# Performance work log

Measured on AMD Instinct MI355X. Metric: run time of the kernel, lower is better.

Reference implementation:

```python
import jax, jax.numpy as jnp
import numpy as np

N_NODES = 50000
N_EDGES = 800000
IN_FEATURES = 256
HIDDEN = 128


def setup_inputs() -> dict:
    key = jax.random.key(0)
    k_x, k_r, k_c, k_v, k_w, k_b = jax.random.split(key, 6)
    x = jax.random.normal(k_x, (N_NODES, IN_FEATURES), dtype=jnp.float32)
    adj_row = jax.random.randint(k_r, (N_EDGES,), 0, N_NODES, dtype=jnp.int32)
    adj_col = jax.random.randint(k_c, (N_EDGES,), 0, N_NODES, dtype=jnp.int32)
    adj_val = jax.random.uniform(k_v, (N_EDGES,), dtype=jnp.float32)
    # Linear params: weight [hidden, in_features] (xavier-normal-ish), bias [hidden]
    std = float(np.sqrt(2.0 / (IN_FEATURES + HIDDEN)))
    W = jax.random.normal(k_w, (HIDDEN, IN_FEATURES), dtype=jnp.float32) * std
    b = jax.random.normal(k_b, (HIDDEN,), dtype=jnp.float32) * 0.01
    return {"x": x, "adj_row": adj_row, "adj_col": adj_col, "adj_val": adj_val, "W": W, "b": b}


def reference(x, adj_row, adj_col, adj_val, W, b):
    # support = Linear(x): [N, hidden]
    support = jnp.einsum('nf,hf->nh', x, W) + b
    # sparse adj @ support via edge-list gather + segment-sum scatter
    gathered = support[adj_col] * adj_val[:, None]          # [E, hidden]
    out = jax.ops.segment_sum(gathered, adj_row, num_segments=N_NODES)  # [N, hidden]
    return out
```

## Files before the change

kernel.cpp:

```cpp
#include <hip/hip_runtime.h>

#define N_NODES 50000
#define N_EDGES 800000
#define IN_F    256
#define HIDDEN  128

#define BUCKET_SZ 64
#define NB        782
#define NBINS     1024
#define EBLOCK    3328
#define EPT       13
#define EBLOCKS   241
#define LIN_ROWS  128
#define LBLOCKS   391
#define NTASKS    632
#define OFSP      784
#define CAP       1300

#define SMEM_BYTES 35840

typedef __attribute__((ext_vector_type(8))) short bf16x8;
typedef __attribute__((ext_vector_type(4))) float f32x4;

__device__ inline unsigned short f2bf(float f) {
    unsigned u = __float_as_uint(f);
    u += 0x7FFF + ((u >> 16) & 1);
    return (unsigned short)(u >> 16);
}
__device__ inline bf16x8 cvt8(float4 a, float4 b) {
    bf16x8 r;
    r[0] = (short)f2bf(a.x); r[1] = (short)f2bf(a.y);
    r[2] = (short)f2bf(a.z); r[3] = (short)f2bf(a.w);
    r[4] = (short)f2bf(b.x); r[5] = (short)f2bf(b.y);
    r[6] = (short)f2bf(b.z); r[7] = (short)f2bf(b.w);
    return r;
}
__device__ inline float bfLo(unsigned u) { return __uint_as_float(u << 16); }
__device__ inline float bfHi(unsigned u) { return __uint_as_float(u & 0xFFFF0000u); }

__global__ __launch_bounds__(256) void fused_linear_partition_kernel(
    const float* __restrict__ x, const float* __restrict__ W,
    const float* __restrict__ bias, unsigned short* __restrict__ support,
    const int* __restrict__ adj_row, const int* __restrict__ adj_col,
    const float* __restrict__ adj_val,
    int2* __restrict__ part, int* __restrict__ ofs)
{
    __shared__ __align__(16) char smem[SMEM_BYTES];
    const int tid = threadIdx.x;

    if (blockIdx.x < EBLOCKS) {
        int2* lbuf = (int2*)smem;
        int*  lofs = (int*)(smem + 26624);
        int*  lcur = (int*)(smem + 30720);
        int*  tsum = (int*)(smem + 34816);

        const int task = blockIdx.x;
        const int base = task * EBLOCK;
        const int n    = min(EBLOCK, N_EDGES - base);

        for (int i = tid; i < NBINS; i += 256) lofs[i] = 0;
        __syncthreads();

        unsigned pk[EPT]; float pv[EPT];
#pragma unroll
        for (int i = 0; i < EPT; ++i) {
            int li = tid + i * 256;
            bool ok = li < n;
            int ee = ok ? (base + li) : base;
            int r = adj_row[ee], c = adj_col[ee];
            float v = adj_val[ee];
            if (ok) {
                unsigned bk = (unsigned)r >> 6;
                pk[i] = (bk << 22) | (((unsigned)r & 63u) << 16) | (unsigned)c;
                pv[i] = v;
                atomicAdd(&lofs[bk], 1);
            } else pk[i] = 0xFFFFFFFFu;
        }
        __syncthreads();

        int s0 = lofs[tid * 4], s1 = lofs[tid * 4 + 1];
        int s2 = lofs[tid * 4 + 2], s3 = lofs[tid * 4 + 3];
        int mysum = s0 + s1 + s2 + s3;
        tsum[tid] = mysum;
        __syncthreads();
#pragma unroll
        for (int off = 1; off < 256; off <<= 1) {
            int t = (tid >= off) ? tsum[tid - off] : 0;
            __syncthreads();
            tsum[tid] += t;
            __syncthreads();
        }
        int ex = tsum[tid] - mysum;
        lofs[tid * 4]     = ex;
        lofs[tid * 4 + 1] = ex + s0;
        lofs[tid * 4 + 2] = ex + s0 + s1;
        lofs[tid * 4 + 3] = ex + s0 + s1 + s2;
        __syncthreads();

        for (int i = tid; i < NBINS; i += 256) lcur[i] = lofs[i];
        __syncthreads();

#pragma unroll
        for (int i = 0; i < EPT; ++i) {
            if (pk[i] != 0xFFFFFFFFu) {
                unsigned bk = pk[i] >> 22;
                int p = atomicAdd(&lcur[bk], 1);
                lbuf[p] = make_int2((int)(pk[i] & 0x3FFFFF), __float_as_int(pv[i]));
            }
        }
        __syncthreads();

        for (int j = tid; j < n; j += 256)
            part[(size_t)task * EBLOCK + j] = lbuf[j];
        for (int i = tid; i <= NB; i += 256)
            ofs[(size_t)task * OFSP + i] = lofs[i];
    } else {
        short* wfrag = (short*)smem;

        const int bid  = blockIdx.x - EBLOCKS;
        const int lane = tid & 63;
        const int wave = tid >> 6;
        const int quad = lane >> 4;
        const int l16  = lane & 15;

        int m0 = bid * LIN_ROWS + wave * 32 + l16;
        int m1 = m0 + 16;
        if (m0 >= N_NODES) m0 = N_NODES - 1;
        if (m1 >= N_NODES) m1 = N_NODES - 1;
        const float* xr0 = x + (size_t)m0 * IN_F;
        const float* xr1 = x + (size_t)m1 * IN_F;

        f32x4 acc[2][8];
#pragma unroll
        for (int g = 0; g < 2; ++g)
#pragma unroll
            for (int s = 0; s < 8; ++s) acc[g][s] = (f32x4){0.f, 0.f, 0.f, 0.f};

#pragma unroll
        for (int half = 0; half < 2; ++half) {
#pragma unroll
            for (int it = 0; it < 8; ++it) {
                const int f   = it * 256 + tid;
                const int ln  = f & 63;
                const int s   = (f >> 6) & 7;
                const int kc  = f >> 9;
                const int row = s * 16 + (ln & 15);
                const int k0  = (half * 4 + kc) * 32 + (ln >> 4) * 8;
                const float* wp = W + (size_t)row * IN_F + k0;
                float4 b0 = *(const float4*)wp;
                float4 b1 = *(const float4*)(wp + 4);
                *(bf16x8*)(&wfrag[(size_t)f * 8]) = cvt8(b0, b1);
            }
            __syncthreads();

#pragma unroll
            for (int kc = 0; kc < 4; ++kc) {
                const int k0 = (half * 4 + kc) * 32 + quad * 8;
                float4 a0 = *(const float4*)(xr0 + k0);
                float4 a1 = *(const float4*)(xr0 + k0 + 4);
                bf16x8 af0 = cvt8(a0, a1);
                float4 a2 = *(const float4*)(xr1 + k0);
                float4 a3 = *(const float4*)(xr1 + k0 + 4);
                bf16x8 af1 = cvt8(a2, a3);
                const short* bbase = &wfrag[((size_t)(kc * 8) * 64 + lane) * 8];
#pragma unroll
                for (int s = 0; s < 8; ++s) {
                    bf16x8 bf = *(const bf16x8*)(bbase + (size_t)s * 64 * 8);
                    acc[0][s] = __builtin_amdgcn_mfma_f32_16x16x32_bf16(af0, bf, acc[0][s], 0, 0, 0);
                    acc[1][s] = __builtin_amdgcn_mfma_f32_16x16x32_bf16(af1, bf, acc[1][s], 0, 0, 0);
                }
            }
            __syncthreads();
        }

#pragma unroll
        for (int g = 0; g < 2; ++g) {
            const int rowBase = bid * LIN_ROWS + wave * 32 + g * 16 + quad * 4;
#pragma unroll
            for (int reg = 0; reg < 4; ++reg) {
                const int r = rowBase + reg;
                if (r < N_NODES) {
#pragma unroll
                    for (int s = 0; s < 8; ++s) {
                        const int col = s * 16 + l16;
                        float v = acc[g][s][reg] + bias[col];
                        support[(size_t)r * HIDDEN + col] = f2bf(v);
                    }
                }
            }
        }
    }
}

__global__ __launch_bounds__(512) void bucket_gather_kernel(
    const int* __restrict__ ofs, const int2* __restrict__ part,
    const unsigned int* __restrict__ support_u32, float* __restrict__ out)
{
    __shared__ int2 sbufA[CAP];
    __shared__ int2 sbufB[CAP];
    __shared__ int  sarr[512];
    __shared__ int  hist[BUCKET_SZ];
    __shared__ int  rp[BUCKET_SZ + 1];
    __shared__ int  cur[BUCKET_SZ];

    const int tid  = threadIdx.x;
    const int b    = blockIdx.x;
    const int wave = tid >> 6;
    const int lane = tid & 63;

    if (tid < BUCKET_SZ) hist[tid] = 0;

    int sstart = 0, slen = 0;
    if (tid < EBLOCKS) {
        const int* orow = ofs + (size_t)tid * OFSP + b;
        sstart = orow[0];
        slen   = orow[1] - sstart;
    }
    sarr[tid] = slen;
    __syncthreads();

#pragma unroll
    for (int off = 1; off < 512; off <<= 1) {
        int t = (tid >= off) ? sarr[tid - off] : 0;
        __syncthreads();
        sarr[tid] += t;
        __syncthreads();
    }
    const int excl = sarr[tid] - slen;
    const int n    = min(sarr[511], CAP);

    {
        const int2* seg = part + (size_t)tid * EBLOCK + sstart;
        for (int k = 0; k < slen; ++k) {
            int p = excl + k;
            if (p < CAP) sbufA[p] = seg[k];
        }
    }
    __syncthreads();

    for (int j = tid; j < n; j += 512)
        atomicAdd(&hist[(sbufA[j].x >> 16) & 63], 1);
    __syncthreads();

    if (tid < 64) {
        int a = hist[tid];
        int ia = a;
#pragma unroll
        for (int off = 1; off < 64; off <<= 1) {
            int t = __shfl_up(ia, off);
            if (tid >= off) ia += t;
        }
        rp[tid + 1] = ia;
        if (tid == 0) rp[0] = 0;
        cur[tid] = ia - a;
    }
    __syncthreads();

    for (int j = tid; j < n; j += 512) {
        int2 cv = sbufA[j];
        int p = atomicAdd(&cur[(cv.x >> 16) & 63], 1);
        sbufB[p] = cv;
    }
    __syncthreads();

    const int rowLo = wave * 8;
#pragma unroll 1
    for (int r = rowLo; r < rowLo + 8; ++r) {
        const int grow = b * BUCKET_SZ + r;
        if (grow >= N_NODES) break;
        const int s = rp[r], e = rp[r + 1];
        float ax = 0.f, ay = 0.f;
        int j = s;
        for (; j + 3 < e; j += 4) {
            int2 c0 = sbufB[j],     c1 = sbufB[j + 1];
            int2 c2 = sbufB[j + 2], c3 = sbufB[j + 3];
            unsigned u0 = support_u32[(size_t)(c0.x & 0xFFFF) * 64 + lane];
            unsigned u1 = support_u32[(size_t)(c1.x & 0xFFFF) * 64 + lane];
            unsigned u2 = support_u32[(size_t)(c2.x & 0xFFFF) * 64 + lane];
            unsigned u3 = support_u32[(size_t)(c3.x & 0xFFFF) * 64 + lane];
            float v0 = __int_as_float(c0.y), v1 = __int_as_float(c1.y);
            float v2 = __int_as_float(c2.y), v3 = __int_as_float(c3.y);
            ax += v0 * bfLo(u0); ay += v0 * bfHi(u0);
            ax += v1 * bfLo(u1); ay += v1 * bfHi(u1);
            ax += v2 * bfLo(u2); ay += v2 * bfHi(u2);
            ax += v3 * bfLo(u3); ay += v3 * bfHi(u3);
        }
        for (; j < e; ++j) {
            int2 cv = sbufB[j];
            unsigned u = support_u32[(size_t)(cv.x & 0xFFFF) * 64 + lane];
            float v = __int_as_float(cv.y);
            ax += v * bfLo(u); ay += v * bfHi(u);
        }
        *(float2*)(out + (size_t)grow * HIDDEN + lane * 2) = make_float2(ax, ay);
    }
}

extern "C" void kernel_launch(void* const* d_in, const int* in_sizes, int n_in,
                              void* d_out, int out_size, void* d_ws, size_t ws_size,
                              hipStream_t stream) {
    const float* x       = (const float*)d_in[0];
    const int*   adj_row = (const int*)d_in[1];
    const int*   adj_col = (const int*)d_in[2];
    const float* adj_val = (const float*)d_in[3];
    const float* W       = (const float*)d_in[4];
    const float* b       = (const float*)d_in[5];
    float* out = (float*)d_out;

    char* wsb = (char*)d_ws;
    const size_t off_support = 0;
    const size_t off_part    = off_support + (size_t)N_NODES * HIDDEN * 2;
    const size_t off_ofs     = off_part + (size_t)EBLOCKS * EBLOCK * 8;

    unsigned short* support = (unsigned short*)(wsb + off_support);
    int2* part = (int2*)(wsb + off_part);
    int*  ofs  = (int*)(wsb + off_ofs);

    fused_linear_partition_kernel<<<NTASKS, 256, 0, stream>>>(
        x, W, b, support, adj_row, adj_col, adj_val, part, ofs);
    bucket_gather_kernel<<<NB, 512, 0, stream>>>(
        ofs, part, (const unsigned int*)support, out);
}
```

Measured before the change: 159.6 us.

## Transpose bucket offsets, use wave-shuffle scan, fuse histogram, unroll gather by 8

The per-block bucket offset table is stored transposed, so the gather kernel reads each bucket's offsets with coalesced loads. The 512-wide shared-memory Hillis-Steele scan, which needed many barriers, is replaced by a wave-level shuffle scan plus a small cross-wave sum. The histogram atomic is folded into the segment copy loop, removing one pass and one barrier. The inner gather gets an 8-way unrolled stage for more memory-level parallelism, at the cost of more registers.

```diff
diff --git a/kernel.cpp b/kernel.cpp
--- a/kernel.cpp
+++ b/kernel.cpp
@@ -14,7 +14,7 @@
 #define LIN_ROWS  128
 #define LBLOCKS   391
 #define NTASKS    632
-#define OFSP      784
+#define OFST_W    256
 #define CAP       1300
 
 #define SMEM_BYTES 35840
@@ -43,7 +43,7 @@
     const float* __restrict__ bias, unsigned short* __restrict__ support,
     const int* __restrict__ adj_row, const int* __restrict__ adj_col,
     const float* __restrict__ adj_val,
-    int2* __restrict__ part, int* __restrict__ ofs)
+    int2* __restrict__ part, int* __restrict__ ofsT)
 {
     __shared__ __align__(16) char smem[SMEM_BYTES];
     const int tid = threadIdx.x;
@@ -113,7 +113,7 @@
         for (int j = tid; j < n; j += 256)
             part[(size_t)task * EBLOCK + j] = lbuf[j];
         for (int i = tid; i <= NB; i += 256)
-            ofs[(size_t)task * OFSP + i] = lofs[i];
+            ofsT[(size_t)i * OFST_W + task] = lofs[i];
     } else {
         short* wfrag = (short*)smem;
 
@@ -193,12 +193,12 @@
 }
 
 __global__ __launch_bounds__(512) void bucket_gather_kernel(
-    const int* __restrict__ ofs, const int2* __restrict__ part,
+    const int* __restrict__ ofsT, const int2* __restrict__ part,
     const unsigned int* __restrict__ support_u32, float* __restrict__ out)
 {
     __shared__ int2 sbufA[CAP];
     __shared__ int2 sbufB[CAP];
-    __shared__ int  sarr[512];
+    __shared__ int  wsum[8];
     __shared__ int  hist[BUCKET_SZ];
     __shared__ int  rp[BUCKET_SZ + 1];
     __shared__ int  cur[BUCKET_SZ];
@@ -210,36 +210,41 @@
 
     if (tid < BUCKET_SZ) hist[tid] = 0;
 
-    int sstart = 0, slen = 0;
+    int s0 = 0, slen = 0;
     if (tid < EBLOCKS) {
-        const int* orow = ofs + (size_t)tid * OFSP + b;
-        sstart = orow[0];
-        slen   = orow[1] - sstart;
-    }
-    sarr[tid] = slen;
+        s0   = ofsT[(size_t)b * OFST_W + tid];
+        slen = ofsT[(size_t)(b + 1) * OFST_W + tid] - s0;
+    }
+
+    int iv = slen;
+#pragma unroll
+    for (int off = 1; off < 64; off <<= 1) {
+        int t = __shfl_up(iv, off);
+        if (lane >= off) iv += t;
+    }
+    if (lane == 63) wsum[wave] = iv;
     __syncthreads();
-
-#pragma unroll
-    for (int off = 1; off < 512; off <<= 1) {
-        int t = (tid >= off) ? sarr[tid - off] : 0;
-        __syncthreads();
-        sarr[tid] += t;
-        __syncthreads();
-    }
-    const int excl = sarr[tid] - slen;
-    const int n    = min(sarr[511], CAP);
+    int wpre = 0, total = 0;
+#pragma unroll
+    for (int w = 0; w < 8; ++w) {
+        int sw = wsum[w];
+        total += sw;
+        if (w < wave) wpre += sw;
+    }
+    const int excl = wpre + iv - slen;
+    const int n    = min(total, CAP);
 
     {
-        const int2* seg = part + (size_t)tid * EBLOCK + sstart;
+        const int2* seg = part + (size_t)tid * EBLOCK + s0;
         for (int k = 0; k < slen; ++k) {
             int p = excl + k;
-            if (p < CAP) sbufA[p] = seg[k];
-        }
-    }
-    __syncthreads();
-
-    for (int j = tid; j < n; j += 512)
-        atomicAdd(&hist[(sbufA[j].x >> 16) & 63], 1);
+            if (p < CAP) {
+                int2 cv = seg[k];
+                sbufA[p] = cv;
+                atomicAdd(&hist[(cv.x >> 16) & 63], 1);
+            }
+        }
+    }
     __syncthreads();
 
     if (tid < 64) {
@@ -271,6 +276,32 @@
         const int s = rp[r], e = rp[r + 1];
         float ax = 0.f, ay = 0.f;
         int j = s;
+        for (; j + 7 < e; j += 8) {
+            int2 c0 = sbufB[j],     c1 = sbufB[j + 1];
+            int2 c2 = sbufB[j + 2], c3 = sbufB[j + 3];
+            int2 c4 = sbufB[j + 4], c5 = sbufB[j + 5];
+            int2 c6 = sbufB[j + 6], c7 = sbufB[j + 7];
+            unsigned u0 = support_u32[(size_t)(c0.x & 0xFFFF) * 64 + lane];
+            unsigned u1 = support_u32[(size_t)(c1.x & 0xFFFF) * 64 + lane];
+            unsigned u2 = support_u32[(size_t)(c2.x & 0xFFFF) * 64 + lane];
+            unsigned u3 = support_u32[(size_t)(c3.x & 0xFFFF) * 64 + lane];
+            unsigned u4 = support_u32[(size_t)(c4.x & 0xFFFF) * 64 + lane];
+            unsigned u5 = support_u32[(size_t)(c5.x & 0xFFFF) * 64 + lane];
+            unsigned u6 = support_u32[(size_t)(c6.x & 0xFFFF) * 64 + lane];
+            unsigned u7 = support_u32[(size_t)(c7.x & 0xFFFF) * 64 + lane];
+            float v0 = __int_as_float(c0.y), v1 = __int_as_float(c1.y);
+            float v2 = __int_as_float(c2.y), v3 = __int_as_float(c3.y);
+            float v4 = __int_as_float(c4.y), v5 = __int_as_float(c5.y);
+            float v6 = __int_as_float(c6.y), v7 = __int_as_float(c7.y);
+            ax += v0 * bfLo(u0); ay += v0 * bfHi(u0);
+            ax += v1 * bfLo(u1); ay += v1 * bfHi(u1);
+            ax += v2 * bfLo(u2); ay += v2 * bfHi(u2);
+            ax += v3 * bfLo(u3); ay += v3 * bfHi(u3);
+            ax += v4 * bfLo(u4); ay += v4 * bfHi(u4);
+            ax += v5 * bfLo(u5); ay += v5 * bfHi(u5);
+            ax += v6 * bfLo(u6); ay += v6 * bfHi(u6);
+            ax += v7 * bfLo(u7); ay += v7 * bfHi(u7);
+        }
         for (; j + 3 < e; j += 4) {
             int2 c0 = sbufB[j],     c1 = sbufB[j + 1];
             int2 c2 = sbufB[j + 2], c3 = sbufB[j + 3];
@@ -309,14 +340,14 @@
     char* wsb = (char*)d_ws;
     const size_t off_support = 0;
     const size_t off_part    = off_support + (size_t)N_NODES * HIDDEN * 2;
-    const size_t off_ofs     = off_part + (size_t)EBLOCKS * EBLOCK * 8;
+    const size_t off_ofsT    = off_part + (size_t)EBLOCKS * EBLOCK * 8;
 
     unsigned short* support = (unsigned short*)(wsb + off_support);
     int2* part = (int2*)(wsb + off_part);
-    int*  ofs  = (int*)(wsb + off_ofs);
+    int*  ofsT = (int*)(wsb + off_ofsT);
 
     fused_linear_partition_kernel<<<NTASKS, 256, 0, stream>>>(
-        x, W, b, support, adj_row, adj_col, adj_val, part, ofs);
+        x, W, b, support, adj_row, adj_col, adj_val, part, ofsT);
     bucket_gather_kernel<<<NB, 512, 0, stream>>>(
-        ofs, part, (const unsigned int*)support, out);
-}
+        ofsT, part, (const unsigned int*)support, out);
+}
```

New measurement: 159.0 us. No clear change (-0.4%).
